# Kernel optimization log

Hardware: AMD Instinct MI355X
Metric: run time of the kernel (lower is better)

Reference implementation:

```python
import jax, jax.numpy as jnp
import numpy as np

DIM = 4096
N_HEADS = 32
N_KV_HEADS = 8
HEAD_DIM = 128
B, S = 2, 2048


def setup_inputs() -> dict:
    key = jax.random.key(0)
    k1, k2, k3, k4, k5 = jax.random.split(key, 5)
    sc = 0.02
    return {
        "x": jax.random.normal(k1, (B, S, DIM), dtype=jnp.float32),
        "wq": jax.random.normal(k2, (N_HEADS * HEAD_DIM, DIM), dtype=jnp.float32) * sc,
        "wk": jax.random.normal(k3, (N_KV_HEADS * HEAD_DIM, DIM), dtype=jnp.float32) * sc,
        "wv": jax.random.normal(k4, (N_KV_HEADS * HEAD_DIM, DIM), dtype=jnp.float32) * sc,
        "wo": jax.random.normal(k5, (DIM, N_HEADS * HEAD_DIM), dtype=jnp.float32) * sc,
    }


def reference(x, wq, wk, wv, wo):
    b, s, _ = x.shape
    groups = N_HEADS // N_KV_HEADS
    # projections (torch Linear: y = x @ W.T)
    q = (x @ wq.T).reshape(b, s, N_HEADS, HEAD_DIM).transpose(0, 2, 1, 3)      # [b,H,s,d]
    k = (x @ wk.T).reshape(b, s, N_KV_HEADS, HEAD_DIM).transpose(0, 2, 1, 3)   # [b,Hkv,s,d]
    v = (x @ wv.T).reshape(b, s, N_KV_HEADS, HEAD_DIM).transpose(0, 2, 1, 3)
    # GQA: attend q grouped per kv head without materializing expanded k/v
    qg = q.reshape(b, N_KV_HEADS, groups, s, HEAD_DIM)                          # [b,Hkv,g,s,d]
    scores = jnp.einsum("bhgqd,bhkd->bhgqk", qg, k) * (HEAD_DIM ** -0.5)
    attn = jax.nn.softmax(scores, axis=-1)                                      # no causal mask (as in source)
    out = jnp.einsum("bhgqk,bhkd->bhgqd", attn, v)                              # [b,Hkv,g,s,d]
    out = out.reshape(b, N_HEADS, s, HEAD_DIM).transpose(0, 2, 1, 3).reshape(b, s, N_HEADS * HEAD_DIM)
    return out @ wo.T
```

## Files before the change

kernel.cpp:

```cpp
#include <hip/hip_runtime.h>
#include <stdint.h>


typedef __attribute__((ext_vector_type(4))) float f32x4;
typedef __attribute__((ext_vector_type(4))) float float4v;
typedef __attribute__((ext_vector_type(8))) short short8;
typedef __attribute__((ext_vector_type(8))) __bf16 bf16x8;
typedef __attribute__((ext_vector_type(4))) unsigned short ushort4v;

#define B_SZ 2
#define S_SZ 2048
#define DIM_SZ 4096
#define NH 32
#define NKV 8
#define HD 128
#define CEXP 0.12752531f

static __device__ __forceinline__ unsigned short f2bf(float f) {
  unsigned int u = __builtin_bit_cast(unsigned int, f);
  u = (u + 0x7fffu + ((u >> 16) & 1u)) >> 16;
  return (unsigned short)u;
}
static __device__ __forceinline__ float bf2f(unsigned short h) {
  unsigned int u = ((unsigned int)h) << 16;
  return __builtin_bit_cast(float, u);
}
static __device__ __forceinline__ f32x4 mfma16(short8 a, short8 b, f32x4 c) {
  return __builtin_amdgcn_mfma_f32_16x16x32_bf16(
      __builtin_bit_cast(bf16x8, a), __builtin_bit_cast(bf16x8, b), c, 0, 0, 0);
}
static __device__ __forceinline__ void gload16(const void* g, void* l) {
  __builtin_amdgcn_global_load_lds(
      (const __attribute__((address_space(1))) unsigned int*)g,
      (__attribute__((address_space(3))) unsigned int*)l, 16, 0, 0);
}

__global__ __launch_bounds__(256) void cvt_kernel(const float* __restrict__ src,
                                                  unsigned short* __restrict__ dst,
                                                  int n4) {
  int i = blockIdx.x * 256 + threadIdx.x;
  if (i >= n4) return;
  float4v v = ((const float4v*)src)[i];
  ushort4v o;
  o[0] = f2bf(v[0]); o[1] = f2bf(v[1]); o[2] = f2bf(v[2]); o[3] = f2bf(v[3]);
  ((ushort4v*)dst)[i] = o;
}

template <int EPI>
__global__ __launch_bounds__(512, 2) void gemm256(const unsigned short* __restrict__ A,
                                                  const unsigned short* __restrict__ B,
                                                  void* __restrict__ Cout,
                                                  int N, int K, int H) {
  __shared__ unsigned short lds[65536];
  const int tid = threadIdx.x;
  const int lane = tid & 63;
  const int wave = tid >> 6;
  const int wm = wave >> 2;
  const int wn = wave & 3;
  const int fr = lane & 15, fg = lane >> 4;
  const int m0 = blockIdx.y * 256, n0 = blockIdx.x * 256;
  const int NT = K >> 6;

  auto seg = [&](int buf, int ab, int half) -> unsigned short* {
    return lds + ((((buf << 1) | ab) << 1) | half) * 8192;
  };

  const int srow = tid >> 3;
  const int scol = ((tid & 7) ^ (srow & 7)) << 3;
  const unsigned short* Abase = A + (size_t)(m0 + srow) * K + scol;
  const unsigned short* Bbase = B + (size_t)(n0 + srow) * K + scol;

  auto stageA = [&](int t, int h) {
    const unsigned short* g = Abase + (size_t)(h * 128) * K + t * 64;
    unsigned short* d = seg(t & 1, 0, h);
    gload16(g, d + tid * 8);
    gload16(g + (size_t)64 * K, d + 4096 + tid * 8);
  };
  auto stageB = [&](int t, int h) {
    const unsigned short* g = Bbase + (size_t)(h * 128) * K + t * 64;
    unsigned short* d = seg(t & 1, 1, h);
    gload16(g, d + tid * 8);
    gload16(g + (size_t)64 * K, d + 4096 + tid * 8);
  };

  f32x4 acc[8][4] = {};

  stageA(0, 0); stageA(0, 1);
  stageB(0, 0); stageB(0, 1);
  stageB(1, 0); stageB(1, 1);
  asm volatile("s_waitcnt vmcnt(4)" ::: "memory");
  __builtin_amdgcn_s_barrier();

#pragma unroll 1
  for (int t = 0; t < NT; ++t) {
    const unsigned short* Aseg = seg(t & 1, 0, wm);
    const unsigned short* Bseg = seg(t & 1, 1, wn >> 1);
    const int brow0 = (wn & 1) * 64;
    short8 aR[4][2], b01[2][2], b23[2][2];

#pragma unroll
    for (int mi = 0; mi < 4; ++mi)
#pragma unroll
      for (int ks = 0; ks < 2; ++ks) {
        const int row = mi * 16 + fr;
        aR[mi][ks] = *(const short8*)&Aseg[row * 64 + ((((ks << 2) + fg) ^ (row & 7)) << 3)];
      }
#pragma unroll
    for (int ni = 0; ni < 2; ++ni)
#pragma unroll
      for (int ks = 0; ks < 2; ++ks) {
        const int row = brow0 + ni * 16 + fr;
        b01[ni][ks] = *(const short8*)&Bseg[row * 64 + ((((ks << 2) + fg) ^ (row & 7)) << 3)];
      }
    if (t + 1 < NT) stageA(t + 1, 0);
    __builtin_amdgcn_sched_barrier(0);
    __builtin_amdgcn_s_barrier();
    asm volatile("s_waitcnt lgkmcnt(0)" ::: "memory");
    __builtin_amdgcn_sched_barrier(0);
    __builtin_amdgcn_s_setprio(1);
#pragma unroll
    for (int mi = 0; mi < 4; ++mi)
#pragma unroll
      for (int ni = 0; ni < 2; ++ni)
#pragma unroll
        for (int ks = 0; ks < 2; ++ks)
          acc[mi][ni] = mfma16(aR[mi][ks], b01[ni][ks], acc[mi][ni]);
    __builtin_amdgcn_s_setprio(0);
    __builtin_amdgcn_sched_barrier(0);
    __builtin_amdgcn_s_barrier();

#pragma unroll
    for (int ni = 0; ni < 2; ++ni)
#pragma unroll
      for (int ks = 0; ks < 2; ++ks) {
        const int row = brow0 + (ni + 2) * 16 + fr;
        b23[ni][ks] = *(const short8*)&Bseg[row * 64 + ((((ks << 2) + fg) ^ (row & 7)) << 3)];
      }
    if (t + 1 < NT) stageA(t + 1, 1);
    __builtin_amdgcn_sched_barrier(0);
    __builtin_amdgcn_s_barrier();
    asm volatile("s_waitcnt lgkmcnt(0)" ::: "memory");
    __builtin_amdgcn_sched_barrier(0);
    __builtin_amdgcn_s_setprio(1);
#pragma unroll
    for (int mi = 0; mi < 4; ++mi)
#pragma unroll
      for (int ni = 0; ni < 2; ++ni)
#pragma unroll
        for (int ks = 0; ks < 2; ++ks)
          acc[mi][ni + 2] = mfma16(aR[mi][ks], b23[ni][ks], acc[mi][ni + 2]);
    __builtin_amdgcn_s_setprio(0);
    __builtin_amdgcn_sched_barrier(0);
    __builtin_amdgcn_s_barrier();

#pragma unroll
    for (int mi = 0; mi < 4; ++mi)
#pragma unroll
      for (int ks = 0; ks < 2; ++ks) {
        const int row = (mi + 4) * 16 + fr;
        aR[mi][ks] = *(const short8*)&Aseg[row * 64 + ((((ks << 2) + fg) ^ (row & 7)) << 3)];
      }
    if (t + 2 < NT) stageB(t + 2, 0);
    __builtin_amdgcn_sched_barrier(0);
    __builtin_amdgcn_s_barrier();
    asm volatile("s_waitcnt lgkmcnt(0)" ::: "memory");
    __builtin_amdgcn_sched_barrier(0);
    __builtin_amdgcn_s_setprio(1);
#pragma unroll
    for (int mi = 0; mi < 4; ++mi)
#pragma unroll
      for (int ni = 0; ni < 2; ++ni)
#pragma unroll
        for (int ks = 0; ks < 2; ++ks)
          acc[mi + 4][ni] = mfma16(aR[mi][ks], b01[ni][ks], acc[mi + 4][ni]);
    __builtin_amdgcn_s_setprio(0);
    __builtin_amdgcn_sched_barrier(0);
    __builtin_amdgcn_s_barrier();

    if (t + 2 < NT) {
      stageB(t + 2, 1);
      __builtin_amdgcn_sched_barrier(0);
      asm volatile("s_waitcnt vmcnt(4)" ::: "memory");
    } else {
      __builtin_amdgcn_sched_barrier(0);
      asm volatile("s_waitcnt vmcnt(0)" ::: "memory");
    }
    __builtin_amdgcn_s_barrier();
    __builtin_amdgcn_s_setprio(1);
#pragma unroll
    for (int mi = 0; mi < 4; ++mi)
#pragma unroll
      for (int ni = 0; ni < 2; ++ni)
#pragma unroll
        for (int ks = 0; ks < 2; ++ks)
          acc[mi + 4][ni + 2] = mfma16(aR[mi][ks], b23[ni][ks], acc[mi + 4][ni + 2]);
    __builtin_amdgcn_s_setprio(0);
    __builtin_amdgcn_sched_barrier(0);
    __builtin_amdgcn_s_barrier();
  }

#pragma unroll
  for (int mi = 0; mi < 8; ++mi) {
#pragma unroll
    for (int ni = 0; ni < 4; ++ni) {
      const int mb = m0 + wm * 128 + mi * 16 + fg * 4;
      const int n = n0 + wn * 64 + ni * 16 + fr;
      if (EPI == 0) {
        float* C = (float*)Cout;
#pragma unroll
        for (int r = 0; r < 4; ++r) C[(size_t)(mb + r) * N + n] = acc[mi][ni][r];
      } else {
        unsigned short* C = (unsigned short*)Cout;
        const int h = n >> 7, d = n & 127;
#pragma unroll
        for (int r = 0; r < 4; ++r) {
          const int m = mb + r;
          const int bb = m >> 11, s = m & 2047;
          C[(((size_t)(bb * H + h)) * S_SZ + s) * HD + d] = f2bf(acc[mi][ni][r]);
        }
      }
    }
  }
}

template <int EPI>
__global__ __launch_bounds__(256) void gemm_bt(const unsigned short* __restrict__ A,
                                               const unsigned short* __restrict__ B,
                                               void* __restrict__ Cout,
                                               void* __restrict__ Cout2,
                                               int N, int K, int H) {
  __shared__ unsigned short As[128 * 32];
  __shared__ unsigned short Bs[128 * 32];
  const int tid = threadIdx.x;
  const int lane = tid & 63;
  const int wave = tid >> 6;
  const int wr = wave >> 1, wc = wave & 1;
  const int m0 = blockIdx.y * 128, n0 = blockIdx.x * 128;

  f32x4 acc[4][4] = {};

  const int srow = tid >> 2;
  const int swz8 = ((tid & 3) ^ (srow & 3)) * 8;
  const unsigned short* Ap0 = A + (size_t)(m0 + srow) * K + swz8;
  const unsigned short* Ap1 = Ap0 + (size_t)64 * K;
  const unsigned short* Bp0 = B + (size_t)(n0 + srow) * K + swz8;
  const unsigned short* Bp1 = Bp0 + (size_t)64 * K;
  unsigned short* Ad0 = As + tid * 8;
  unsigned short* Ad1 = As + 2048 + tid * 8;
  unsigned short* Bd0 = Bs + tid * 8;
  unsigned short* Bd1 = Bs + 2048 + tid * 8;

  const int fr = lane & 15;
  const int fg = lane >> 4;
  const int rsl = (fg ^ (fr & 3)) * 8;

#pragma unroll 1
  for (int kt = 0; kt < K; kt += 32) {
    gload16(Ap0 + kt, Ad0);
    gload16(Ap1 + kt, Ad1);
    gload16(Bp0 + kt, Bd0);
    gload16(Bp1 + kt, Bd1);
    __syncthreads();
    short8 a[4], b[4];
#pragma unroll
    for (int i = 0; i < 4; i++)
      a[i] = *(const short8*)&As[(wr * 64 + i * 16 + fr) * 32 + rsl];
#pragma unroll
    for (int i = 0; i < 4; i++)
      b[i] = *(const short8*)&Bs[(wc * 64 + i * 16 + fr) * 32 + rsl];
#pragma unroll
    for (int mi = 0; mi < 4; mi++)
#pragma unroll
      for (int ni = 0; ni < 4; ni++)
        acc[mi][ni] = mfma16(a[mi], b[ni], acc[mi][ni]);
    __syncthreads();
  }

#pragma unroll
  for (int mi = 0; mi < 4; mi++) {
#pragma unroll
    for (int ni = 0; ni < 4; ni++) {
      const int mb = m0 + wr * 64 + mi * 16 + fg * 4;
      const int n = n0 + wc * 64 + ni * 16 + fr;
      if (EPI == 0) {
        float* C = (float*)Cout;
#pragma unroll
        for (int r = 0; r < 4; r++) C[(size_t)(mb + r) * N + n] = acc[mi][ni][r];
      } else if (EPI == 1) {
        unsigned short* C = (unsigned short*)Cout;
        const int h = n >> 7, d = n & 127;
#pragma unroll
        for (int r = 0; r < 4; r++) {
          const int m = mb + r;
          const int bb = m >> 11, s = m & 2047;
          C[(((size_t)(bb * H + h)) * S_SZ + s) * HD + d] = f2bf(acc[mi][ni][r]);
        }
      } else if (EPI == 3) {
        if (n < 1024) {
          unsigned short* C = (unsigned short*)Cout;
          const int h = n >> 7, d = n & 127;
#pragma unroll
          for (int r = 0; r < 4; r++) {
            const int m = mb + r;
            const int bb = m >> 11, s = m & 2047;
            C[(((size_t)(bb * NKV + h)) * S_SZ + s) * HD + d] = f2bf(acc[mi][ni][r]);
          }
        } else {
          unsigned short* C = (unsigned short*)Cout2;
          const int vr = n - 1024;
          const int h = vr >> 7, d = vr & 127;
          const int bb = mb >> 11, s = mb & 2047;
          ushort4v pk;
#pragma unroll
          for (int r = 0; r < 4; r++) pk[r] = f2bf(acc[mi][ni][r]);
          *(ushort4v*)&C[(((size_t)(bb * NKV + h)) * HD + d) * S_SZ + s] = pk;
        }
      }
    }
  }
}

__global__ __launch_bounds__(256) void attn_kernel(const unsigned short* __restrict__ Q,
                                                   const unsigned short* __restrict__ Kg,
                                                   const unsigned short* __restrict__ Vt,
                                                   unsigned short* __restrict__ AO) {
  __shared__ unsigned short Ks[64 * 128];
  __shared__ unsigned short Vs[128 * 64];
  __shared__ unsigned short Ps[4][16 * 72];
  const int tid = threadIdx.x, lane = tid & 63, wave = tid >> 6;
  const int qt = blockIdx.x, h = blockIdx.y, b = blockIdx.z;
  const int hk = h >> 2;
  const size_t qbase = ((size_t)(b * NH + h) * S_SZ) * HD;
  const size_t kbase = ((size_t)(b * NKV + hk) * S_SZ) * HD;
  const size_t vbase = ((size_t)(b * NKV + hk) * HD) * S_SZ;
  const int q0 = qt * 64 + wave * 16;
  const int fr = lane & 15, fg = lane >> 4;

  short8 qf[4];
#pragma unroll
  for (int dc = 0; dc < 4; dc++)
    qf[dc] = *(const short8*)&Q[qbase + (size_t)(q0 + fr) * HD + dc * 32 + fg * 8];

  f32x4 acco[8] = {};
  float m_r[4], l_r[4];
#pragma unroll
  for (int r = 0; r < 4; r++) { m_r[r] = -3.0e38f; l_r[r] = 0.f; }

  const int krow = tid >> 4, kslot = tid & 15;
  const int vrow = tid >> 3, vslot = tid & 7;

#pragma unroll 1
  for (int kt = 0; kt < S_SZ; kt += 64) {
#pragma unroll
    for (int i = 0; i < 4; i++) {
      const int row = i * 16 + krow;
      const int c = kslot ^ (row & 7);
      gload16(&Kg[kbase + (size_t)(kt + row) * HD + c * 8], &Ks[i * 2048 + tid * 8]);
    }
#pragma unroll
    for (int i = 0; i < 4; i++) {
      const int row = i * 32 + vrow;
      const int c = vslot ^ (row & 7);
      gload16(&Vt[vbase + (size_t)row * S_SZ + kt + c * 8], &Vs[i * 2048 + tid * 8]);
    }
    __syncthreads();

    f32x4 sf[4] = {};
#pragma unroll
    for (int kb = 0; kb < 4; kb++) {
      const int row = kb * 16 + fr;
#pragma unroll
      for (int dc = 0; dc < 4; dc++) {
        const int slot = (dc * 4 + fg) ^ (row & 7);
        short8 kf = *(const short8*)&Ks[row * 128 + slot * 8];
        sf[kb] = mfma16(qf[dc], kf, sf[kb]);
      }
    }

#pragma unroll
    for (int r = 0; r < 4; r++) {
      float tmax = fmaxf(fmaxf(sf[0][r], sf[1][r]), fmaxf(sf[2][r], sf[3][r]));
      tmax = fmaxf(tmax, __shfl_xor(tmax, 1));
      tmax = fmaxf(tmax, __shfl_xor(tmax, 2));
      tmax = fmaxf(tmax, __shfl_xor(tmax, 4));
      tmax = fmaxf(tmax, __shfl_xor(tmax, 8));
      const float mnew = fmaxf(m_r[r], tmax);
      const float alpha = __builtin_amdgcn_exp2f((m_r[r] - mnew) * CEXP);
      m_r[r] = mnew;
      float ps = 0.f;
      const int prow = fg * 4 + r;
#pragma unroll
      for (int kb = 0; kb < 4; kb++) {
        const unsigned short pb = f2bf(__builtin_amdgcn_exp2f((sf[kb][r] - mnew) * CEXP));
        ps += bf2f(pb);
        Ps[wave][prow * 72 + kb * 16 + fr] = pb;
      }
      ps += __shfl_xor(ps, 1);
      ps += __shfl_xor(ps, 2);
      ps += __shfl_xor(ps, 4);
      ps += __shfl_xor(ps, 8);
      l_r[r] = l_r[r] * alpha + ps;
#pragma unroll
      for (int dt = 0; dt < 8; dt++) acco[dt][r] *= alpha;
    }

    short8 pf[2];
#pragma unroll
    for (int kc = 0; kc < 2; kc++)
      pf[kc] = *(const short8*)&Ps[wave][fr * 72 + kc * 32 + fg * 8];
#pragma unroll
    for (int dt = 0; dt < 8; dt++) {
      const int row = dt * 16 + fr;
#pragma unroll
      for (int kc = 0; kc < 2; kc++) {
        const int slot = (kc * 4 + fg) ^ (row & 7);
        short8 vf = *(const short8*)&Vs[row * 64 + slot * 8];
        acco[dt] = mfma16(pf[kc], vf, acco[dt]);
      }
    }
    __syncthreads();
  }

#pragma unroll
  for (int r = 0; r < 4; r++) {
    const float inv = 1.0f / l_r[r];
    const int s = q0 + fg * 4 + r;
    const size_t ob = (((size_t)(b * S_SZ + s)) * NH + h) * HD;
#pragma unroll
    for (int dt = 0; dt < 8; dt++)
      AO[ob + dt * 16 + fr] = f2bf(acco[dt][r] * inv);
  }
}

extern "C" void kernel_launch(void* const* d_in, const int* in_sizes, int n_in,
                              void* d_out, int out_size, void* d_ws, size_t ws_size,
                              hipStream_t stream) {
  const float* x  = (const float*)d_in[0];
  const float* wq = (const float*)d_in[1];
  const float* wk = (const float*)d_in[2];
  const float* wv = (const float*)d_in[3];
  const float* wo = (const float*)d_in[4];

  unsigned short* ws = (unsigned short*)d_ws;
  const size_t SZ_BIG = (size_t)DIM_SZ * DIM_SZ;
  const size_t SZ_SMALL = (size_t)(NKV * HD) * DIM_SZ;
  unsigned short* xb   = ws;
  unsigned short* wbig = xb + SZ_BIG;
  unsigned short* wkb  = wbig + SZ_BIG;
  unsigned short* wvb  = wkb + SZ_SMALL;
  unsigned short* Qb   = wvb + SZ_SMALL;
  unsigned short* Kb   = Qb + SZ_BIG;
  unsigned short* Vtb  = Kb + SZ_SMALL;
  unsigned short* AOb  = Vtb + SZ_SMALL;

  cvt_kernel<<<16384, 256, 0, stream>>>(x, xb, 4194304);
  cvt_kernel<<<16384, 256, 0, stream>>>(wq, wbig, 4194304);
  cvt_kernel<<<4096, 256, 0, stream>>>(wk, wkb, 1048576);
  cvt_kernel<<<4096, 256, 0, stream>>>(wv, wvb, 1048576);

  gemm256<1><<<dim3(16, 16), 512, 0, stream>>>(xb, wbig, Qb, 4096, DIM_SZ, NH);
  gemm_bt<3><<<dim3(16, 32), 256, 0, stream>>>(xb, wkb, Kb, Vtb, 2048, DIM_SZ, NKV);

  attn_kernel<<<dim3(32, 32, 2), 256, 0, stream>>>(Qb, Kb, Vtb, AOb);

  cvt_kernel<<<16384, 256, 0, stream>>>(wo, wbig, 4194304);
  gemm256<0><<<dim3(16, 16), 512, 0, stream>>>(AOb, wbig, d_out, 4096, DIM_SZ, NH);
}
```

Before: 869.6 us.

## Rewrite attention with 32x32 MFMA, register-resident P, double-buffered K/V and lazy rescale

Result: faster. 744.2 us (-14.4%).

```diff
diff --git a/kernel.cpp b/kernel.cpp
--- a/kernel.cpp
+++ b/kernel.cpp
@@ -3,10 +3,12 @@
 
 
 typedef __attribute__((ext_vector_type(4))) float f32x4;
+typedef __attribute__((ext_vector_type(16))) float f32x16;
 typedef __attribute__((ext_vector_type(4))) float float4v;
 typedef __attribute__((ext_vector_type(8))) short short8;
 typedef __attribute__((ext_vector_type(8))) __bf16 bf16x8;
 typedef __attribute__((ext_vector_type(4))) unsigned short ushort4v;
+typedef __attribute__((ext_vector_type(4))) unsigned int uint4v;
 
 #define B_SZ 2
 #define S_SZ 2048
@@ -21,18 +23,23 @@
   u = (u + 0x7fffu + ((u >> 16) & 1u)) >> 16;
   return (unsigned short)u;
 }
-static __device__ __forceinline__ float bf2f(unsigned short h) {
-  unsigned int u = ((unsigned int)h) << 16;
-  return __builtin_bit_cast(float, u);
-}
 static __device__ __forceinline__ f32x4 mfma16(short8 a, short8 b, f32x4 c) {
   return __builtin_amdgcn_mfma_f32_16x16x32_bf16(
+      __builtin_bit_cast(bf16x8, a), __builtin_bit_cast(bf16x8, b), c, 0, 0, 0);
+}
+static __device__ __forceinline__ f32x16 mfma32(short8 a, short8 b, f32x16 c) {
+  return __builtin_amdgcn_mfma_f32_32x32x16_bf16(
       __builtin_bit_cast(bf16x8, a), __builtin_bit_cast(bf16x8, b), c, 0, 0, 0);
 }
 static __device__ __forceinline__ void gload16(const void* g, void* l) {
   __builtin_amdgcn_global_load_lds(
       (const __attribute__((address_space(1))) unsigned int*)g,
       (__attribute__((address_space(3))) unsigned int*)l, 16, 0, 0);
+}
+static __device__ __forceinline__ unsigned int cvtpk(float lo, float hi) {
+  unsigned int r;
+  asm("v_cvt_pk_bf16_f32 %0, %1, %2" : "=v"(r) : "v"(lo), "v"(hi));
+  return r;
 }
 
 __global__ __launch_bounds__(256) void cvt_kernel(const float* __restrict__ src,
@@ -286,15 +293,6 @@
         float* C = (float*)Cout;
 #pragma unroll
         for (int r = 0; r < 4; r++) C[(size_t)(mb + r) * N + n] = acc[mi][ni][r];
-      } else if (EPI == 1) {
-        unsigned short* C = (unsigned short*)Cout;
-        const int h = n >> 7, d = n & 127;
-#pragma unroll
-        for (int r = 0; r < 4; r++) {
-          const int m = mb + r;
-          const int bb = m >> 11, s = m & 2047;
-          C[(((size_t)(bb * H + h)) * S_SZ + s) * HD + d] = f2bf(acc[mi][ni][r]);
-        }
       } else if (EPI == 3) {
         if (n < 1024) {
           unsigned short* C = (unsigned short*)Cout;
@@ -320,116 +318,144 @@
   }
 }
 
-__global__ __launch_bounds__(256) void attn_kernel(const unsigned short* __restrict__ Q,
+__global__ __launch_bounds__(512) void attn_kernel(const unsigned short* __restrict__ Q,
                                                    const unsigned short* __restrict__ Kg,
                                                    const unsigned short* __restrict__ Vt,
                                                    unsigned short* __restrict__ AO) {
-  __shared__ unsigned short Ks[64 * 128];
-  __shared__ unsigned short Vs[128 * 64];
-  __shared__ unsigned short Ps[4][16 * 72];
-  const int tid = threadIdx.x, lane = tid & 63, wave = tid >> 6;
-  const int qt = blockIdx.x, h = blockIdx.y, b = blockIdx.z;
-  const int hk = h >> 2;
-  const size_t qbase = ((size_t)(b * NH + h) * S_SZ) * HD;
+  __shared__ unsigned short Ks[2][64 * 128];
+  __shared__ unsigned short Vs[2][128 * 64];
+  const int tid = threadIdx.x, lane = tid & 63, w = tid >> 6;
+  const int l31 = lane & 31, h = lane >> 5;
+  const int qt = blockIdx.x, hq = blockIdx.y, b = blockIdx.z;
+  const int hk = hq >> 2;
+  const size_t qbase = ((size_t)(b * NH + hq) * S_SZ) * HD;
   const size_t kbase = ((size_t)(b * NKV + hk) * S_SZ) * HD;
   const size_t vbase = ((size_t)(b * NKV + hk) * HD) * S_SZ;
-  const int q0 = qt * 64 + wave * 16;
-  const int fr = lane & 15, fg = lane >> 4;
-
-  short8 qf[4];
-#pragma unroll
-  for (int dc = 0; dc < 4; dc++)
-    qf[dc] = *(const short8*)&Q[qbase + (size_t)(q0 + fr) * HD + dc * 32 + fg * 8];
-
-  f32x4 acco[8] = {};
-  float m_r[4], l_r[4];
-#pragma unroll
-  for (int r = 0; r < 4; r++) { m_r[r] = -3.0e38f; l_r[r] = 0.f; }
-
-  const int krow = tid >> 4, kslot = tid & 15;
-  const int vrow = tid >> 3, vslot = tid & 7;
+  const int q = qt * 256 + w * 32 + l31;
+
+  short8 qf[8];
+#pragma unroll
+  for (int c = 0; c < 8; ++c)
+    qf[c] = *(const short8*)&Q[qbase + (size_t)q * HD + c * 16 + h * 8];
+
+  const int p0 = tid, p1 = tid + 512;
+  const int kr0 = p0 >> 4, kc0 = ((p0 & 15) ^ (kr0 & 7)) << 3;
+  const int kr1 = p1 >> 4, kc1 = ((p1 & 15) ^ (kr1 & 7)) << 3;
+  const int vr0 = p0 >> 3, vc0 = ((p0 & 7) ^ (vr0 & 7)) << 3;
+  const int vr1 = p1 >> 3, vc1 = ((p1 & 7) ^ (vr1 & 7)) << 3;
+
+  auto stage = [&](int bufi, int kt) {
+    gload16(&Kg[kbase + (size_t)(kt + kr0) * HD + kc0], &Ks[bufi][p0 * 8]);
+    gload16(&Kg[kbase + (size_t)(kt + kr1) * HD + kc1], &Ks[bufi][p1 * 8]);
+    gload16(&Vt[vbase + (size_t)vr0 * S_SZ + kt + vc0], &Vs[bufi][p0 * 8]);
+    gload16(&Vt[vbase + (size_t)vr1 * S_SZ + kt + vc1], &Vs[bufi][p1 * 8]);
+  };
+
+  f32x16 ao[4] = {};
+  float m_r = -3.0e38f, l_r = 0.f;
+
+  stage(0, 0);
+  asm volatile("s_waitcnt vmcnt(0)" ::: "memory");
+  __syncthreads();
 
 #pragma unroll 1
-  for (int kt = 0; kt < S_SZ; kt += 64) {
-#pragma unroll
-    for (int i = 0; i < 4; i++) {
-      const int row = i * 16 + krow;
-      const int c = kslot ^ (row & 7);
-      gload16(&Kg[kbase + (size_t)(kt + row) * HD + c * 8], &Ks[i * 2048 + tid * 8]);
-    }
-#pragma unroll
-    for (int i = 0; i < 4; i++) {
-      const int row = i * 32 + vrow;
-      const int c = vslot ^ (row & 7);
-      gload16(&Vt[vbase + (size_t)row * S_SZ + kt + c * 8], &Vs[i * 2048 + tid * 8]);
-    }
-    __syncthreads();
-
-    f32x4 sf[4] = {};
-#pragma unroll
-    for (int kb = 0; kb < 4; kb++) {
-      const int row = kb * 16 + fr;
-#pragma unroll
-      for (int dc = 0; dc < 4; dc++) {
-        const int slot = (dc * 4 + fg) ^ (row & 7);
-        short8 kf = *(const short8*)&Ks[row * 128 + slot * 8];
-        sf[kb] = mfma16(qf[dc], kf, sf[kb]);
-      }
-    }
-
-#pragma unroll
-    for (int r = 0; r < 4; r++) {
-      float tmax = fmaxf(fmaxf(sf[0][r], sf[1][r]), fmaxf(sf[2][r], sf[3][r]));
-      tmax = fmaxf(tmax, __shfl_xor(tmax, 1));
-      tmax = fmaxf(tmax, __shfl_xor(tmax, 2));
-      tmax = fmaxf(tmax, __shfl_xor(tmax, 4));
-      tmax = fmaxf(tmax, __shfl_xor(tmax, 8));
-      const float mnew = fmaxf(m_r[r], tmax);
-      const float alpha = __builtin_amdgcn_exp2f((m_r[r] - mnew) * CEXP);
-      m_r[r] = mnew;
-      float ps = 0.f;
-      const int prow = fg * 4 + r;
-#pragma unroll
-      for (int kb = 0; kb < 4; kb++) {
-        const unsigned short pb = f2bf(__builtin_amdgcn_exp2f((sf[kb][r] - mnew) * CEXP));
-        ps += bf2f(pb);
-        Ps[wave][prow * 72 + kb * 16 + fr] = pb;
-      }
-      ps += __shfl_xor(ps, 1);
-      ps += __shfl_xor(ps, 2);
-      ps += __shfl_xor(ps, 4);
-      ps += __shfl_xor(ps, 8);
-      l_r[r] = l_r[r] * alpha + ps;
-#pragma unroll
-      for (int dt = 0; dt < 8; dt++) acco[dt][r] *= alpha;
-    }
-
-    short8 pf[2];
-#pragma unroll
-    for (int kc = 0; kc < 2; kc++)
-      pf[kc] = *(const short8*)&Ps[wave][fr * 72 + kc * 32 + fg * 8];
-#pragma unroll
-    for (int dt = 0; dt < 8; dt++) {
-      const int row = dt * 16 + fr;
-#pragma unroll
-      for (int kc = 0; kc < 2; kc++) {
-        const int slot = (kc * 4 + fg) ^ (row & 7);
-        short8 vf = *(const short8*)&Vs[row * 64 + slot * 8];
-        acco[dt] = mfma16(pf[kc], vf, acco[dt]);
-      }
-    }
+  for (int t = 0; t < 32; ++t) {
+    const int cur = t & 1;
+    if (t + 1 < 32) stage(cur ^ 1, (t + 1) * 64);
+    const unsigned short* K_ = Ks[cur];
+    const unsigned short* V_ = Vs[cur];
+
+    f32x16 sf[2] = {};
+#pragma unroll
+    for (int kb = 0; kb < 2; ++kb) {
+      const int row = kb * 32 + l31;
+#pragma unroll
+      for (int c = 0; c < 8; ++c) {
+        const int ch = (c * 2 + h) ^ (row & 7);
+        short8 kf = *(const short8*)&K_[row * 128 + ch * 8];
+        sf[kb] = mfma32(kf, qf[c], sf[kb]);
+      }
+    }
+
+    float tm = sf[0][0];
+#pragma unroll
+    for (int r = 1; r < 16; ++r) tm = fmaxf(tm, sf[0][r]);
+#pragma unroll
+    for (int r = 0; r < 16; ++r) tm = fmaxf(tm, sf[1][r]);
+    tm = fmaxf(tm, __shfl_xor(tm, 32));
+
+    const bool skip = ((tm - m_r) * CEXP <= 8.0f);
+    if (!__all(skip)) {
+      const float mnew = fmaxf(m_r, tm);
+      const float al = __builtin_amdgcn_exp2f((m_r - mnew) * CEXP);
+      l_r *= al;
+#pragma unroll
+      for (int db = 0; db < 4; ++db)
+#pragma unroll
+        for (int r = 0; r < 16; ++r) ao[db][r] *= al;
+      m_r = mnew;
+    }
+
+    const float nmc = -m_r * CEXP;
+    float p[2][16];
+    float ps = 0.f;
+#pragma unroll
+    for (int kb = 0; kb < 2; ++kb)
+#pragma unroll
+      for (int r = 0; r < 16; ++r) {
+        p[kb][r] = __builtin_amdgcn_exp2f(fmaf(sf[kb][r], CEXP, nmc));
+        ps += p[kb][r];
+      }
+    ps += __shfl_xor(ps, 32);
+    l_r += ps;
+
+    uint4v pw[4];
+#pragma unroll
+    for (int kb = 0; kb < 2; ++kb)
+#pragma unroll
+      for (int hs = 0; hs < 2; ++hs) {
+        const int f = kb * 2 + hs;
+        const unsigned int X  = cvtpk(p[kb][hs * 8 + 0], p[kb][hs * 8 + 1]);
+        const unsigned int X2 = cvtpk(p[kb][hs * 8 + 2], p[kb][hs * 8 + 3]);
+        const unsigned int Y  = cvtpk(p[kb][hs * 8 + 4], p[kb][hs * 8 + 5]);
+        const unsigned int Y2 = cvtpk(p[kb][hs * 8 + 6], p[kb][hs * 8 + 7]);
+        const unsigned int xs  = __shfl_xor(X, 32);
+        const unsigned int xs2 = __shfl_xor(X2, 32);
+        const unsigned int ys  = __shfl_xor(Y, 32);
+        const unsigned int ys2 = __shfl_xor(Y2, 32);
+        pw[f][0] = h ? ys : X;
+        pw[f][1] = h ? ys2 : X2;
+        pw[f][2] = h ? Y : xs;
+        pw[f][3] = h ? Y2 : xs2;
+      }
+
+#pragma unroll
+    for (int db = 0; db < 4; ++db) {
+      const int row = db * 32 + l31;
+#pragma unroll
+      for (int f = 0; f < 4; ++f) {
+        const int ch = (f * 2 + h) ^ (row & 7);
+        short8 vf = *(const short8*)&V_[row * 64 + ch * 8];
+        ao[db] = mfma32(vf, __builtin_bit_cast(short8, pw[f]), ao[db]);
+      }
+    }
+
+    asm volatile("s_waitcnt vmcnt(0)" ::: "memory");
     __syncthreads();
   }
 
-#pragma unroll
-  for (int r = 0; r < 4; r++) {
-    const float inv = 1.0f / l_r[r];
-    const int s = q0 + fg * 4 + r;
-    const size_t ob = (((size_t)(b * S_SZ + s)) * NH + h) * HD;
-#pragma unroll
-    for (int dt = 0; dt < 8; dt++)
-      AO[ob + dt * 16 + fr] = f2bf(acco[dt][r] * inv);
-  }
+  const float inv = 1.0f / l_r;
+  const size_t ob = (((size_t)(b * S_SZ + q)) * NH + hq) * HD;
+#pragma unroll
+  for (int db = 0; db < 4; ++db)
+#pragma unroll
+    for (int rg = 0; rg < 4; ++rg) {
+      const int d0 = db * 32 + rg * 8 + h * 4;
+      ushort4v pk;
+#pragma unroll
+      for (int j = 0; j < 4; ++j) pk[j] = f2bf(ao[db][rg * 4 + j] * inv);
+      *(ushort4v*)&AO[ob + d0] = pk;
+    }
 }
 
 extern "C" void kernel_launch(void* const* d_in, const int* in_sizes, int n_in,
@@ -461,7 +487,7 @@
   gemm256<1><<<dim3(16, 16), 512, 0, stream>>>(xb, wbig, Qb, 4096, DIM_SZ, NH);
   gemm_bt<3><<<dim3(16, 32), 256, 0, stream>>>(xb, wkb, Kb, Vtb, 2048, DIM_SZ, NKV);
 
-  attn_kernel<<<dim3(32, 32, 2), 256, 0, stream>>>(Qb, Kb, Vtb, AOb);
+  attn_kernel<<<dim3(8, 32, 2), 512, 0, stream>>>(Qb, Kb, Vtb, AOb);
 
   cvt_kernel<<<16384, 256, 0, stream>>>(wo, wbig, 4194304);
   gemm256<0><<<dim3(16, 16), 512, 0, stream>>>(AOb, wbig, d_out, 4096, DIM_SZ, NH);
```
